# Optimization experiments

Hardware: AMD Instinct MI355X
Metric: run time of the kernel (lower is better)

## Reference

```python
import jax, jax.numpy as jnp
import numpy as np

DIM = 1024
NHEADS = 16
DIM_HEAD = 64
HIDDEN = NHEADS * DIM_HEAD  # 1024


def _xavier(key, fan_in, fan_out):
    limit = np.sqrt(6.0 / (fan_in + fan_out))
    return jax.random.uniform(key, (fan_in, fan_out), jnp.float32, -limit, limit)


def setup_inputs() -> dict:
    key = jax.random.key(0)
    kq, k1, k2, k3 = jax.random.split(key, 4)
    q = jax.random.normal(kq, (2, 2048, DIM), jnp.float32)
    Wq = _xavier(k1, DIM, HIDDEN)
    bq = jnp.zeros((HIDDEN,), jnp.float32)
    Wkv = _xavier(k2, DIM, 2 * HIDDEN)
    bkv = jnp.zeros((2 * HIDDEN,), jnp.float32)
    Wo = _xavier(k3, HIDDEN, DIM)
    bo = jnp.zeros((DIM,), jnp.float32)
    return {"q": q, "Wq": Wq, "bq": bq, "Wkv": Wkv, "bkv": bkv, "Wo": Wo, "bo": bo}


def reference(q, Wq, bq, Wkv, bkv, Wo, bo):
    scale = DIM_HEAD ** (-0.5)
    query = q @ Wq + bq                      # [b, s, hidden]
    kv = q @ Wkv + bkv                       # self-attention: kv from q
    key_, value = jnp.split(kv, 2, axis=-1)  # [b, s, hidden] each
    b, s, _ = query.shape
    query = query.reshape(b, s, NHEADS, DIM_HEAD)
    key_ = key_.reshape(b, s, NHEADS, DIM_HEAD)
    value = value.reshape(b, s, NHEADS, DIM_HEAD)
    scores = jnp.einsum('bqhd,bkhd->bhqk', query, key_) * scale
    attn = jax.nn.softmax(scores, axis=-1)
    out = jnp.einsum('bhqk,bkhd->bqhd', attn, value)
    out = out.reshape(b, s, HIDDEN)
    return out @ Wo + bo
```

## Files before the change

### kernel.cpp

```cpp
#include <hip/hip_runtime.h>

#define DIM 1024
#define NHEADS 16
#define DH 64
#define BATCH 2
#define SEQ 2048

typedef float f32x4 __attribute__((ext_vector_type(4)));
typedef short s16x8 __attribute__((ext_vector_type(8)));
typedef short s16x4 __attribute__((ext_vector_type(4)));

__device__ __forceinline__ short f2bf(float f) {
    union { float f; unsigned u; } v; v.f = f;
    unsigned r = v.u + 0x7fffu + ((v.u >> 16) & 1u);
    return (short)(r >> 16);
}

#if defined(__has_builtin)
#if __has_builtin(__builtin_amdgcn_cvt_pk_bf16_f32)
#define HAVE_PK_BF16 1
#endif
#endif
__device__ __forceinline__ unsigned f2bf_pk(float a, float b) {
#ifdef HAVE_PK_BF16
    typedef __bf16 bf16x2_t __attribute__((ext_vector_type(2)));
    bf16x2_t r = __builtin_amdgcn_cvt_pk_bf16_f32(a, b);
    return __builtin_bit_cast(unsigned, r);
#else
    return ((unsigned)(unsigned short)f2bf(b) << 16) | (unsigned short)f2bf(a);
#endif
}
__device__ __forceinline__ s16x4 pk4(float a, float b, float c, float d) {
    union { unsigned u[2]; s16x4 v; } x;
    x.u[0] = f2bf_pk(a, b); x.u[1] = f2bf_pk(c, d);
    return x.v;
}

#if defined(__has_builtin)
#if __has_builtin(__builtin_amdgcn_exp2f)
#define EXP2(x) __builtin_amdgcn_exp2f(x)
#endif
#endif
#ifndef EXP2
#define EXP2(x) exp2f(x)
#endif

__device__ __forceinline__ void gld16(const void* g, void* l) {
    __builtin_amdgcn_global_load_lds(
        (const __attribute__((address_space(1))) void*)g,
        (__attribute__((address_space(3))) void*)l, 16, 0, 0);
}

__global__ __launch_bounds__(256) void convert_bf16_kernel(
    const float* __restrict__ X, short* __restrict__ Y)
{
    const int i = (blockIdx.x * 256 + threadIdx.x) * 8;
    float4 a = *(const float4*)(X + i);
    float4 b = *(const float4*)(X + i + 4);
    union { unsigned u[4]; s16x8 v; } o;
    o.u[0] = f2bf_pk(a.x, a.y); o.u[1] = f2bf_pk(a.z, a.w);
    o.u[2] = f2bf_pk(b.x, b.y); o.u[3] = f2bf_pk(b.z, b.w);
    *(s16x8*)(Y + i) = o.v;
}

__global__ __launch_bounds__(256) void transpose_w_kernel(
    const float* __restrict__ Wq, const float* __restrict__ Wkv,
    const float* __restrict__ Wo, short* __restrict__ WT)
{
    const int t  = threadIdx.x;
    const int ng = blockIdx.x * 64 + (t & 63);
    const int k0 = (blockIdx.y * 4 + (t >> 6)) * 8;
    const float* W; int n, N;
    if (ng < 1024)      { W = Wq;  n = ng;        N = 1024; }
    else if (ng < 3072) { W = Wkv; n = ng - 1024; N = 2048; }
    else                { W = Wo;  n = ng - 3072; N = 1024; }
    float v[8];
#pragma unroll
    for (int j = 0; j < 8; ++j) v[j] = W[(size_t)(k0 + j) * N + n];
    union { unsigned u[4]; s16x8 s; } o;
    o.u[0] = f2bf_pk(v[0], v[1]); o.u[1] = f2bf_pk(v[2], v[3]);
    o.u[2] = f2bf_pk(v[4], v[5]); o.u[3] = f2bf_pk(v[6], v[7]);
    *(s16x8*)&WT[(size_t)ng * 1024 + k0] = o.s;
}

__global__ __launch_bounds__(256) void transpose_v_kernel(
    const short* __restrict__ QKV, short* __restrict__ VtG)
{
    const int t = threadIdx.x;
    const int tok0 = blockIdx.x * 64;
    const int h = blockIdx.y, b = blockIdx.z;
    __shared__ short L[64 * 72];
    const short* src = QKV + (size_t)(b * SEQ + tok0) * 3072 + 2048 + h * 64;
#pragma unroll
    for (int p = 0; p < 2; ++p) {
        int r = p * 32 + (t >> 3);
        *(s16x8*)&L[r * 72 + (t & 7) * 8] = *(const s16x8*)(src + (size_t)r * 3072 + (t & 7) * 8);
    }
    __syncthreads();
    short* dst = VtG + (size_t)(b * NHEADS + h) * 64 * SEQ + tok0;
#pragma unroll
    for (int p = 0; p < 2; ++p) {
        int u = p * 256 + t;
        int dv = u >> 3, c = (u & 7) * 8;
        s16x8 o;
#pragma unroll
        for (int j = 0; j < 8; ++j) o[j] = L[(c + j) * 72 + dv];
        *(s16x8*)(dst + (size_t)dv * SEQ + c) = o;
    }
}

template<int TM, bool OUT_BF16>
__global__ __launch_bounds__(256) void gemm_mfma_kernel(
    const short* __restrict__ A, const short* __restrict__ Bt,
    const float* __restrict__ bias0, const float* __restrict__ bias1, int nsplit,
    float s0, float s1, void* __restrict__ C, int M, int N)
{
    const int K = 1024;
    constexpr int NI = (TM == 128) ? 4 : 2;
    __shared__ short As[TM * 32];
    __shared__ short Bs[128 * 32];

    const int t    = threadIdx.x;
    const int wave = t >> 6;
    const int lane = t & 63;
    const int col  = lane & 15;
    const int quad = lane >> 4;
    const int m0 = blockIdx.y * TM;
    const int n0 = blockIdx.x * 128;
    const int wroff = (TM == 128) ? (wave >> 1) * 64 : 0;
    const int wcoff = (TM == 128) ? (wave & 1) * 64 : wave * 32;

    f32x4 acc[4][NI];
#pragma unroll
    for (int mi = 0; mi < 4; ++mi)
#pragma unroll
        for (int ni = 0; ni < NI; ++ni) acc[mi][ni] = (f32x4){0.f, 0.f, 0.f, 0.f};

    constexpr int RPW = TM / 4;
    const int ldrowA = wave * RPW + (lane >> 2);
    const int ldrowB = wave * 32  + (lane >> 2);
    const int ldcol  = (lane & 3) * 8;
    const short* Ag = A  + (size_t)(m0 + ldrowA) * K + ldcol;
    const short* Bg = Bt + (size_t)(n0 + ldrowB) * K + ldcol;
    short* AsW = &As[wave * RPW * 32];
    short* BsW = &Bs[wave * 1024];

    for (int k0 = 0; k0 < K; k0 += 32) {
        __syncthreads();
        gld16(Ag + k0, AsW);
        if (TM == 128) gld16(Ag + 16 * K + k0, AsW + 512);
        gld16(Bg + k0,          BsW);
        gld16(Bg + 16 * K + k0, BsW + 512);
        __syncthreads();

        s16x8 aA[4], bB[NI];
#pragma unroll
        for (int mi = 0; mi < 4; ++mi)
            aA[mi] = *(const s16x8*)&As[(wroff + 16 * mi + col) * 32 + quad * 8];
#pragma unroll
        for (int ni = 0; ni < NI; ++ni)
            bB[ni] = *(const s16x8*)&Bs[(wcoff + 16 * ni + col) * 32 + quad * 8];
#pragma unroll
        for (int mi = 0; mi < 4; ++mi)
#pragma unroll
            for (int ni = 0; ni < NI; ++ni)
                acc[mi][ni] = __builtin_amdgcn_mfma_f32_16x16x32_bf16(aA[mi], bB[ni], acc[mi][ni], 0, 0, 0);
    }

    float bias_v[NI], scale_v[NI];
#pragma unroll
    for (int ni = 0; ni < NI; ++ni) {
        int nb = n0 + wcoff + 16 * ni + col;
        bias_v[ni]  = (nb < nsplit) ? bias0[nb] : bias1[nb - nsplit];
        scale_v[ni] = (nb < nsplit) ? s0 : s1;
    }

#pragma unroll
    for (int mi = 0; mi < 4; ++mi)
#pragma unroll
        for (int ni = 0; ni < NI; ++ni)
#pragma unroll
            for (int r = 0; r < 4; ++r) {
                const int gm = m0 + wroff + 16 * mi + quad * 4 + r;
                const int gn = n0 + wcoff + 16 * ni + col;
                float v = (acc[mi][ni][r] + bias_v[ni]) * scale_v[ni];
                if (OUT_BF16) ((short*)C)[(size_t)gm * N + gn] = f2bf(v);
                else          ((float*)C)[(size_t)gm * N + gn] = v;
            }
}

__global__ __launch_bounds__(512, 4) void attn_v7_kernel(
    const short* __restrict__ QKV,
    const short* __restrict__ VtG,
    short* __restrict__ O)
{
    const int qt = blockIdx.x;
    const int h  = blockIdx.y;
    const int b  = blockIdx.z;
    const int t  = threadIdx.x;
    const int wave = t >> 6;
    const int lane = t & 63;
    const int col  = lane & 15;
    const int quad = lane >> 4;
    const int wq = wave & 3;
    const int kh = wave >> 2;

    __shared__ __align__(16) short L[28672];
    short* KsB = L;
    short* VtB = L + 2 * 64 * 72;
    short* PsW = L + 4 * 64 * 72 + wave * (32 * 40);

    const short* Qg = QKV + (size_t)(b * SEQ + qt * 128) * 3072 + h * DH;
    const short* Kg = QKV + (size_t)(b * SEQ) * 3072 + 1024 + h * DH;
    const short* VtRow = VtG + (size_t)(b * NHEADS + h) * 64 * SEQ;

    s16x8 aQ[2][2];
#pragma unroll
    for (int tq = 0; tq < 2; ++tq)
#pragma unroll
        for (int kq = 0; kq < 2; ++kq)
            aQ[tq][kq] = *(const s16x8*)(Qg + (size_t)(wq * 32 + 16 * tq + col) * 3072 + kq * 32 + quad * 8);

    f32x4 oa[4][2];
    float lsum[2] = {0.f, 0.f};
#pragma unroll
    for (int td = 0; td < 4; ++td)
#pragma unroll
        for (int tq = 0; tq < 2; ++tq) oa[td][tq] = (f32x4){0.f, 0.f, 0.f, 0.f};

    const int srow = t >> 3;
    const int sc8  = (t & 7) * 8;
    const short* KgS  = Kg + (size_t)srow * 3072 + sc8;
    const short* VtgS = VtRow + (size_t)srow * SEQ + sc8;
    s16x8 kx = *(const s16x8*)KgS;
    s16x8 vx = *(const s16x8*)VtgS;

    for (int kt = 0; kt < SEQ / 64; ++kt) {
        const int cur = kt & 1;
        *(s16x8*)&KsB[cur * 4608 + srow * 72 + sc8] = kx;
        *(s16x8*)&VtB[cur * 4608 + srow * 72 + sc8] = vx;
        {
            int nt = (kt + 1 < SEQ / 64) ? kt + 1 : kt;
            kx = *(const s16x8*)(KgS + (size_t)nt * 64 * 3072);
            vx = *(const s16x8*)(VtgS + (size_t)nt * 64);
        }
        __syncthreads();

        s16x8 aK[2][2];
#pragma unroll
        for (int tk = 0; tk < 2; ++tk)
#pragma unroll
            for (int kq = 0; kq < 2; ++kq)
                aK[tk][kq] = *(const s16x8*)&KsB[cur * 4608 + (kh * 32 + 16 * tk + col) * 72 + kq * 32 + quad * 8];
        f32x4 st[2][2];
        __builtin_amdgcn_s_setprio(1);
#pragma unroll
        for (int tk = 0; tk < 2; ++tk)
#pragma unroll
            for (int tq = 0; tq < 2; ++tq) {
                f32x4 a = (f32x4){0.f, 0.f, 0.f, 0.f};
                a = __builtin_amdgcn_mfma_f32_16x16x32_bf16(aK[tk][0], aQ[tq][0], a, 0, 0, 0);
                a = __builtin_amdgcn_mfma_f32_16x16x32_bf16(aK[tk][1], aQ[tq][1], a, 0, 0, 0);
                st[tk][tq] = a;
            }
        __builtin_amdgcn_s_setprio(0);

#pragma unroll
        for (int tk = 0; tk < 2; ++tk)
#pragma unroll
            for (int tq = 0; tq < 2; ++tq) {
                float p0 = EXP2(st[tk][tq][0]);
                float p1 = EXP2(st[tk][tq][1]);
                float p2 = EXP2(st[tk][tq][2]);
                float p3 = EXP2(st[tk][tq][3]);
                lsum[tq] += (p0 + p1) + (p2 + p3);
                *(s16x4*)&PsW[(16 * tq + col) * 40 + 16 * tk + quad * 4] = pk4(p0, p1, p2, p3);
            }
        asm volatile("s_waitcnt lgkmcnt(0)" ::: "memory");

        s16x8 bP[2];
#pragma unroll
        for (int tq = 0; tq < 2; ++tq)
            bP[tq] = *(const s16x8*)&PsW[(16 * tq + col) * 40 + quad * 8];
        __builtin_amdgcn_s_setprio(1);
#pragma unroll
        for (int td = 0; td < 4; ++td) {
            const int dv = 16 * td + col;
            s16x8 aV = *(const s16x8*)&VtB[cur * 4608 + dv * 72 + kh * 32 + quad * 8];
#pragma unroll
            for (int tq = 0; tq < 2; ++tq)
                oa[td][tq] = __builtin_amdgcn_mfma_f32_16x16x32_bf16(aV, bP[tq], oa[td][tq], 0, 0, 0);
        }
        __builtin_amdgcn_s_setprio(0);
    }

#pragma unroll
    for (int tq = 0; tq < 2; ++tq) {
        lsum[tq] += __shfl_xor(lsum[tq], 16);
        lsum[tq] += __shfl_xor(lsum[tq], 32);
    }

    __syncthreads();
    float* red  = (float*)L;
    float* redl = red + 4 * 64 * 36;
    if (wave >= 4) {
        const int slot = wave & 3;
#pragma unroll
        for (int td = 0; td < 4; ++td)
#pragma unroll
            for (int tq = 0; tq < 2; ++tq)
#pragma unroll
                for (int r = 0; r < 4; ++r)
                    red[slot * 2304 + (16 * td + quad * 4 + r) * 36 + 16 * tq + col] = oa[td][tq][r];
        if (quad == 0)
#pragma unroll
            for (int tq = 0; tq < 2; ++tq)
                redl[slot * 32 + 16 * tq + col] = lsum[tq];
    }
    __syncthreads();

    if (wave < 4) {
        const int slot = wq;
#pragma unroll
        for (int td = 0; td < 4; ++td)
#pragma unroll
            for (int tq = 0; tq < 2; ++tq)
#pragma unroll
                for (int r = 0; r < 4; ++r)
                    oa[td][tq][r] += red[slot * 2304 + (16 * td + quad * 4 + r) * 36 + 16 * tq + col];
        float inv[2];
#pragma unroll
        for (int tq = 0; tq < 2; ++tq) {
            lsum[tq] += redl[slot * 32 + 16 * tq + col];
            inv[tq] = 1.f / lsum[tq];
        }
        short* Og = O + (size_t)(b * SEQ + qt * 128 + wq * 32) * DIM + h * DH;
#pragma unroll
        for (int td = 0; td < 4; ++td)
#pragma unroll
            for (int tq = 0; tq < 2; ++tq)
                *(s16x4*)(Og + (size_t)(16 * tq + col) * DIM + 16 * td + quad * 4) =
                    pk4(oa[td][tq][0] * inv[tq], oa[td][tq][1] * inv[tq],
                        oa[td][tq][2] * inv[tq], oa[td][tq][3] * inv[tq]);
    }
}

extern "C" void kernel_launch(void* const* d_in, const int* in_sizes, int n_in,
                              void* d_out, int out_size, void* d_ws, size_t ws_size,
                              hipStream_t stream)
{
    const float* q   = (const float*)d_in[0];
    const float* Wq  = (const float*)d_in[1];
    const float* bq  = (const float*)d_in[2];
    const float* Wkv = (const float*)d_in[3];
    const float* bkv = (const float*)d_in[4];
    const float* Wo  = (const float*)d_in[5];
    const float* bo  = (const float*)d_in[6];
    float* out = (float*)d_out;

    const int M = BATCH * SEQ;

    short* qb     = (short*)d_ws;
    short* WT     = qb     + (size_t)M * DIM;
    short* QKVbuf = WT     + (size_t)4096 * DIM;
    short* AObuf  = QKVbuf + (size_t)M * 3 * DIM;
    short* VtG    = (short*)d_out;

    const float QSCALE = 0.18033688011112042f;

    convert_bf16_kernel<<<(M * DIM) / (256 * 8), 256, 0, stream>>>(q, qb);
    transpose_w_kernel<<<dim3(64, 32), 256, 0, stream>>>(Wq, Wkv, Wo, WT);

    gemm_mfma_kernel<128, true><<<dim3(3 * DIM / 128, M / 128), 256, 0, stream>>>(
        qb, WT, bq, bkv, DIM, QSCALE, 1.0f, QKVbuf, M, 3 * DIM);
    transpose_v_kernel<<<dim3(SEQ / 64, NHEADS, BATCH), 256, 0, stream>>>(QKVbuf, VtG);
    attn_v7_kernel<<<dim3(SEQ / 128, NHEADS, BATCH), 512, 0, stream>>>(QKVbuf, VtG, AObuf);
    gemm_mfma_kernel<64, false><<<dim3(DIM / 128, M / 64), 256, 0, stream>>>(
        AObuf, WT + (size_t)3072 * 1024, bo, bo, 1 << 30, 1.0f, 1.0f, out, M, DIM);
}
```

Baseline: 199.7 us.

## Fuse V transpose into QKV GEMM epilogue, merge prep kernels, remap attention blocks

Merges the input conversion and weight transpose into one prep kernel and removes the separate V-transpose kernel. The QKV GEMM epilogue now writes V columns straight into the transposed per-head layout with 4-element packed stores. The attention grid is remapped so each XCD handles a contiguous set of (batch, head) pairs, which is meant to improve L2 reuse of K/V. The goals are fewer launches, less global traffic, and better cache locality. The cost is strided transposed stores from the GEMM epilogue.

Result: slower. 203.8 us (+2.0%).

```diff
diff --git a/kernel.cpp b/kernel.cpp
--- a/kernel.cpp
+++ b/kernel.cpp
@@ -51,69 +51,44 @@
         (__attribute__((address_space(3))) void*)l, 16, 0, 0);
 }
 
-__global__ __launch_bounds__(256) void convert_bf16_kernel(
-    const float* __restrict__ X, short* __restrict__ Y)
-{
-    const int i = (blockIdx.x * 256 + threadIdx.x) * 8;
-    float4 a = *(const float4*)(X + i);
-    float4 b = *(const float4*)(X + i + 4);
-    union { unsigned u[4]; s16x8 v; } o;
-    o.u[0] = f2bf_pk(a.x, a.y); o.u[1] = f2bf_pk(a.z, a.w);
-    o.u[2] = f2bf_pk(b.x, b.y); o.u[3] = f2bf_pk(b.z, b.w);
-    *(s16x8*)(Y + i) = o.v;
-}
-
-__global__ __launch_bounds__(256) void transpose_w_kernel(
+__global__ __launch_bounds__(256) void prep_kernel(
+    const float* __restrict__ X, short* __restrict__ Y,
     const float* __restrict__ Wq, const float* __restrict__ Wkv,
     const float* __restrict__ Wo, short* __restrict__ WT)
 {
-    const int t  = threadIdx.x;
-    const int ng = blockIdx.x * 64 + (t & 63);
-    const int k0 = (blockIdx.y * 4 + (t >> 6)) * 8;
-    const float* W; int n, N;
-    if (ng < 1024)      { W = Wq;  n = ng;        N = 1024; }
-    else if (ng < 3072) { W = Wkv; n = ng - 1024; N = 2048; }
-    else                { W = Wo;  n = ng - 3072; N = 1024; }
-    float v[8];
-#pragma unroll
-    for (int j = 0; j < 8; ++j) v[j] = W[(size_t)(k0 + j) * N + n];
-    union { unsigned u[4]; s16x8 s; } o;
-    o.u[0] = f2bf_pk(v[0], v[1]); o.u[1] = f2bf_pk(v[2], v[3]);
-    o.u[2] = f2bf_pk(v[4], v[5]); o.u[3] = f2bf_pk(v[6], v[7]);
-    *(s16x8*)&WT[(size_t)ng * 1024 + k0] = o.s;
-}
-
-__global__ __launch_bounds__(256) void transpose_v_kernel(
-    const short* __restrict__ QKV, short* __restrict__ VtG)
-{
     const int t = threadIdx.x;
-    const int tok0 = blockIdx.x * 64;
-    const int h = blockIdx.y, b = blockIdx.z;
-    __shared__ short L[64 * 72];
-    const short* src = QKV + (size_t)(b * SEQ + tok0) * 3072 + 2048 + h * 64;
-#pragma unroll
-    for (int p = 0; p < 2; ++p) {
-        int r = p * 32 + (t >> 3);
-        *(s16x8*)&L[r * 72 + (t & 7) * 8] = *(const s16x8*)(src + (size_t)r * 3072 + (t & 7) * 8);
-    }
-    __syncthreads();
-    short* dst = VtG + (size_t)(b * NHEADS + h) * 64 * SEQ + tok0;
-#pragma unroll
-    for (int p = 0; p < 2; ++p) {
-        int u = p * 256 + t;
-        int dv = u >> 3, c = (u & 7) * 8;
-        s16x8 o;
-#pragma unroll
-        for (int j = 0; j < 8; ++j) o[j] = L[(c + j) * 72 + dv];
-        *(s16x8*)(dst + (size_t)dv * SEQ + c) = o;
-    }
-}
-
-template<int TM, bool OUT_BF16>
+    if (blockIdx.x < 2048) {
+        const int i = (blockIdx.x * 256 + t) * 8;
+        float4 a = *(const float4*)(X + i);
+        float4 b = *(const float4*)(X + i + 4);
+        union { unsigned u[4]; s16x8 v; } o;
+        o.u[0] = f2bf_pk(a.x, a.y); o.u[1] = f2bf_pk(a.z, a.w);
+        o.u[2] = f2bf_pk(b.x, b.y); o.u[3] = f2bf_pk(b.z, b.w);
+        *(s16x8*)(Y + i) = o.v;
+    } else {
+        const int i2 = blockIdx.x - 2048;
+        const int bx = i2 & 63, by = i2 >> 6;
+        const int ng = bx * 64 + (t & 63);
+        const int k0 = (by * 4 + (t >> 6)) * 8;
+        const float* W; int n, N;
+        if (ng < 1024)      { W = Wq;  n = ng;        N = 1024; }
+        else if (ng < 3072) { W = Wkv; n = ng - 1024; N = 2048; }
+        else                { W = Wo;  n = ng - 3072; N = 1024; }
+        float v[8];
+#pragma unroll
+        for (int j = 0; j < 8; ++j) v[j] = W[(size_t)(k0 + j) * N + n];
+        union { unsigned u[4]; s16x8 s; } o;
+        o.u[0] = f2bf_pk(v[0], v[1]); o.u[1] = f2bf_pk(v[2], v[3]);
+        o.u[2] = f2bf_pk(v[4], v[5]); o.u[3] = f2bf_pk(v[6], v[7]);
+        *(s16x8*)&WT[(size_t)ng * 1024 + k0] = o.s;
+    }
+}
+
+template<int TM, bool OUT_BF16, bool FUSE_V>
 __global__ __launch_bounds__(256) void gemm_mfma_kernel(
     const short* __restrict__ A, const short* __restrict__ Bt,
     const float* __restrict__ bias0, const float* __restrict__ bias1, int nsplit,
-    float s0, float s1, void* __restrict__ C, int M, int N)
+    float s0, float s1, void* __restrict__ C, short* __restrict__ VtGp, int M, int N)
 {
     const int K = 1024;
     constexpr int NI = (TM == 128) ? 4 : 2;
@@ -176,27 +151,44 @@
     }
 
 #pragma unroll
-    for (int mi = 0; mi < 4; ++mi)
-#pragma unroll
-        for (int ni = 0; ni < NI; ++ni)
-#pragma unroll
-            for (int r = 0; r < 4; ++r) {
-                const int gm = m0 + wroff + 16 * mi + quad * 4 + r;
-                const int gn = n0 + wcoff + 16 * ni + col;
-                float v = (acc[mi][ni][r] + bias_v[ni]) * scale_v[ni];
-                if (OUT_BF16) ((short*)C)[(size_t)gm * N + gn] = f2bf(v);
-                else          ((float*)C)[(size_t)gm * N + gn] = v;
+    for (int mi = 0; mi < 4; ++mi) {
+        const int gm0 = m0 + wroff + 16 * mi + quad * 4;
+#pragma unroll
+        for (int ni = 0; ni < NI; ++ni) {
+            const int nb_lo = n0 + wcoff + 16 * ni;
+            if (FUSE_V && nb_lo >= 2048) {
+                const int dv = nb_lo - 2048 + col;
+                float v0 = (acc[mi][ni][0] + bias_v[ni]) * scale_v[ni];
+                float v1 = (acc[mi][ni][1] + bias_v[ni]) * scale_v[ni];
+                float v2 = (acc[mi][ni][2] + bias_v[ni]) * scale_v[ni];
+                float v3 = (acc[mi][ni][3] + bias_v[ni]) * scale_v[ni];
+                const int row = ((gm0 >> 11) * NHEADS + (dv >> 6)) * 64 + (dv & 63);
+                *(s16x4*)&VtGp[(size_t)row * SEQ + (gm0 & 2047)] = pk4(v0, v1, v2, v3);
+            } else {
+#pragma unroll
+                for (int r = 0; r < 4; ++r) {
+                    const int gm = gm0 + r;
+                    const int gn = nb_lo + col;
+                    float v = (acc[mi][ni][r] + bias_v[ni]) * scale_v[ni];
+                    if (OUT_BF16) ((short*)C)[(size_t)gm * N + gn] = f2bf(v);
+                    else          ((float*)C)[(size_t)gm * N + gn] = v;
+                }
             }
-}
-
-__global__ __launch_bounds__(512, 4) void attn_v7_kernel(
+        }
+    }
+}
+
+__global__ __launch_bounds__(512, 4) void attn_v9_kernel(
     const short* __restrict__ QKV,
     const short* __restrict__ VtG,
     short* __restrict__ O)
 {
-    const int qt = blockIdx.x;
-    const int h  = blockIdx.y;
-    const int b  = blockIdx.z;
+    const int L = blockIdx.x + 16 * blockIdx.y + 256 * blockIdx.z;
+    const int xcd = L & 7, idx = L >> 3;
+    const int pair = xcd * 4 + (idx >> 4);
+    const int qt = idx & 15;
+    const int h  = pair & 15;
+    const int b  = pair >> 4;
     const int t  = threadIdx.x;
     const int wave = t >> 6;
     const int lane = t & 63;
@@ -205,10 +197,10 @@
     const int wq = wave & 3;
     const int kh = wave >> 2;
 
-    __shared__ __align__(16) short L[28672];
-    short* KsB = L;
-    short* VtB = L + 2 * 64 * 72;
-    short* PsW = L + 4 * 64 * 72 + wave * (32 * 40);
+    __shared__ __align__(16) short Lds[28672];
+    short* KsB = Lds;
+    short* VtB = Lds + 2 * 64 * 72;
+    short* PsW = Lds + 4 * 64 * 72 + wave * (32 * 40);
 
     const short* Qg = QKV + (size_t)(b * SEQ + qt * 128) * 3072 + h * DH;
     const short* Kg = QKV + (size_t)(b * SEQ) * 3072 + 1024 + h * DH;
@@ -301,7 +293,7 @@
     }
 
     __syncthreads();
-    float* red  = (float*)L;
+    float* red  = (float*)Lds;
     float* redl = red + 4 * 64 * 36;
     if (wave >= 4) {
         const int slot = wave & 3;
@@ -368,13 +360,11 @@
 
     const float QSCALE = 0.18033688011112042f;
 
-    convert_bf16_kernel<<<(M * DIM) / (256 * 8), 256, 0, stream>>>(q, qb);
-    transpose_w_kernel<<<dim3(64, 32), 256, 0, stream>>>(Wq, Wkv, Wo, WT);
-
-    gemm_mfma_kernel<128, true><<<dim3(3 * DIM / 128, M / 128), 256, 0, stream>>>(
-        qb, WT, bq, bkv, DIM, QSCALE, 1.0f, QKVbuf, M, 3 * DIM);
-    transpose_v_kernel<<<dim3(SEQ / 64, NHEADS, BATCH), 256, 0, stream>>>(QKVbuf, VtG);
-    attn_v7_kernel<<<dim3(SEQ / 128, NHEADS, BATCH), 512, 0, stream>>>(QKVbuf, VtG, AObuf);
-    gemm_mfma_kernel<64, false><<<dim3(DIM / 128, M / 64), 256, 0, stream>>>(
-        AObuf, WT + (size_t)3072 * 1024, bo, bo, 1 << 30, 1.0f, 1.0f, out, M, DIM);
-}
+    prep_kernel<<<4096, 256, 0, stream>>>(q, qb, Wq, Wkv, Wo, WT);
+
+    gemm_mfma_kernel<128, true, true><<<dim3(3 * DIM / 128, M / 128), 256, 0, stream>>>(
+        qb, WT, bq, bkv, DIM, QSCALE, 1.0f, QKVbuf, VtG, M, 3 * DIM);
+    attn_v9_kernel<<<dim3(SEQ / 128, NHEADS, BATCH), 512, 0, stream>>>(QKVbuf, VtG, AObuf);
+    gemm_mfma_kernel<64, false, false><<<dim3(DIM / 128, M / 64), 256, 0, stream>>>(
+        AObuf, WT + (size_t)3072 * 1024, bo, bo, 1 << 30, 1.0f, 1.0f, out, nullptr, M, DIM);
+}
```

## Fuse prep kernels, single-buffer attention LDS, raise occupancy, remap blocks per XCD

Applied to the files above, without the earlier changes.

The input conversion and weight transpose kernels are merged into one launch to save a kernel launch. The attention kernel drops double-buffered K/V LDS tiles and uses a single buffer guarded by two barriers per tile. This cuts LDS per block so launch bounds can ask for 8 waves per SIMD instead of 4. Block indices are remapped so that each XCD handles a contiguous set of (batch, head) pairs, which should improve L2 reuse of K/V, at the cost of the extra barrier per iteration and tighter register limits.

Result: slower. 434.3 us (+117.4%).

```diff
diff --git a/kernel.cpp b/kernel.cpp
--- a/kernel.cpp
+++ b/kernel.cpp
@@ -51,36 +51,37 @@
         (__attribute__((address_space(3))) void*)l, 16, 0, 0);
 }
 
-__global__ __launch_bounds__(256) void convert_bf16_kernel(
-    const float* __restrict__ X, short* __restrict__ Y)
-{
-    const int i = (blockIdx.x * 256 + threadIdx.x) * 8;
-    float4 a = *(const float4*)(X + i);
-    float4 b = *(const float4*)(X + i + 4);
-    union { unsigned u[4]; s16x8 v; } o;
-    o.u[0] = f2bf_pk(a.x, a.y); o.u[1] = f2bf_pk(a.z, a.w);
-    o.u[2] = f2bf_pk(b.x, b.y); o.u[3] = f2bf_pk(b.z, b.w);
-    *(s16x8*)(Y + i) = o.v;
-}
-
-__global__ __launch_bounds__(256) void transpose_w_kernel(
+__global__ __launch_bounds__(256) void prep_kernel(
+    const float* __restrict__ X, short* __restrict__ Y,
     const float* __restrict__ Wq, const float* __restrict__ Wkv,
     const float* __restrict__ Wo, short* __restrict__ WT)
 {
-    const int t  = threadIdx.x;
-    const int ng = blockIdx.x * 64 + (t & 63);
-    const int k0 = (blockIdx.y * 4 + (t >> 6)) * 8;
-    const float* W; int n, N;
-    if (ng < 1024)      { W = Wq;  n = ng;        N = 1024; }
-    else if (ng < 3072) { W = Wkv; n = ng - 1024; N = 2048; }
-    else                { W = Wo;  n = ng - 3072; N = 1024; }
-    float v[8];
-#pragma unroll
-    for (int j = 0; j < 8; ++j) v[j] = W[(size_t)(k0 + j) * N + n];
-    union { unsigned u[4]; s16x8 s; } o;
-    o.u[0] = f2bf_pk(v[0], v[1]); o.u[1] = f2bf_pk(v[2], v[3]);
-    o.u[2] = f2bf_pk(v[4], v[5]); o.u[3] = f2bf_pk(v[6], v[7]);
-    *(s16x8*)&WT[(size_t)ng * 1024 + k0] = o.s;
+    const int t = threadIdx.x;
+    if (blockIdx.x < 2048) {
+        const int i = (blockIdx.x * 256 + t) * 8;
+        float4 a = *(const float4*)(X + i);
+        float4 b = *(const float4*)(X + i + 4);
+        union { unsigned u[4]; s16x8 v; } o;
+        o.u[0] = f2bf_pk(a.x, a.y); o.u[1] = f2bf_pk(a.z, a.w);
+        o.u[2] = f2bf_pk(b.x, b.y); o.u[3] = f2bf_pk(b.z, b.w);
+        *(s16x8*)(Y + i) = o.v;
+    } else {
+        const int i2 = blockIdx.x - 2048;
+        const int bx = i2 & 63, by = i2 >> 6;
+        const int ng = bx * 64 + (t & 63);
+        const int k0 = (by * 4 + (t >> 6)) * 8;
+        const float* W; int n, N;
+        if (ng < 1024)      { W = Wq;  n = ng;        N = 1024; }
+        else if (ng < 3072) { W = Wkv; n = ng - 1024; N = 2048; }
+        else                { W = Wo;  n = ng - 3072; N = 1024; }
+        float v[8];
+#pragma unroll
+        for (int j = 0; j < 8; ++j) v[j] = W[(size_t)(k0 + j) * N + n];
+        union { unsigned u[4]; s16x8 s; } o;
+        o.u[0] = f2bf_pk(v[0], v[1]); o.u[1] = f2bf_pk(v[2], v[3]);
+        o.u[2] = f2bf_pk(v[4], v[5]); o.u[3] = f2bf_pk(v[6], v[7]);
+        *(s16x8*)&WT[(size_t)ng * 1024 + k0] = o.s;
+    }
 }
 
 __global__ __launch_bounds__(256) void transpose_v_kernel(
@@ -189,14 +190,17 @@
             }
 }
 
-__global__ __launch_bounds__(512, 4) void attn_v7_kernel(
+__global__ __launch_bounds__(512, 8) void attn_v10_kernel(
     const short* __restrict__ QKV,
     const short* __restrict__ VtG,
     short* __restrict__ O)
 {
-    const int qt = blockIdx.x;
-    const int h  = blockIdx.y;
-    const int b  = blockIdx.z;
+    const int L = blockIdx.x + 16 * blockIdx.y + 256 * blockIdx.z;
+    const int xcd = L & 7, idx = L >> 3;
+    const int pair = xcd * 4 + (idx >> 4);
+    const int qt = idx & 15;
+    const int h  = pair & 15;
+    const int b  = pair >> 4;
     const int t  = threadIdx.x;
     const int wave = t >> 6;
     const int lane = t & 63;
@@ -205,10 +209,10 @@
     const int wq = wave & 3;
     const int kh = wave >> 2;
 
-    __shared__ __align__(16) short L[28672];
-    short* KsB = L;
-    short* VtB = L + 2 * 64 * 72;
-    short* PsW = L + 4 * 64 * 72 + wave * (32 * 40);
+    __shared__ __align__(16) short Lds[19456];
+    short* Ks  = Lds;
+    short* Vt  = Lds + 4608;
+    short* PsW = Lds + 9216 + wave * (32 * 40);
 
     const short* Qg = QKV + (size_t)(b * SEQ + qt * 128) * 3072 + h * DH;
     const short* Kg = QKV + (size_t)(b * SEQ) * 3072 + 1024 + h * DH;
@@ -236,22 +240,22 @@
     s16x8 vx = *(const s16x8*)VtgS;
 
     for (int kt = 0; kt < SEQ / 64; ++kt) {
-        const int cur = kt & 1;
-        *(s16x8*)&KsB[cur * 4608 + srow * 72 + sc8] = kx;
-        *(s16x8*)&VtB[cur * 4608 + srow * 72 + sc8] = vx;
+        __syncthreads();
+        *(s16x8*)&Ks[srow * 72 + sc8] = kx;
+        *(s16x8*)&Vt[srow * 72 + sc8] = vx;
+        __syncthreads();
         {
             int nt = (kt + 1 < SEQ / 64) ? kt + 1 : kt;
             kx = *(const s16x8*)(KgS + (size_t)nt * 64 * 3072);
             vx = *(const s16x8*)(VtgS + (size_t)nt * 64);
         }
-        __syncthreads();
 
         s16x8 aK[2][2];
 #pragma unroll
         for (int tk = 0; tk < 2; ++tk)
 #pragma unroll
             for (int kq = 0; kq < 2; ++kq)
-                aK[tk][kq] = *(const s16x8*)&KsB[cur * 4608 + (kh * 32 + 16 * tk + col) * 72 + kq * 32 + quad * 8];
+                aK[tk][kq] = *(const s16x8*)&Ks[(kh * 32 + 16 * tk + col) * 72 + kq * 32 + quad * 8];
         f32x4 st[2][2];
         __builtin_amdgcn_s_setprio(1);
 #pragma unroll
@@ -286,7 +290,7 @@
 #pragma unroll
         for (int td = 0; td < 4; ++td) {
             const int dv = 16 * td + col;
-            s16x8 aV = *(const s16x8*)&VtB[cur * 4608 + dv * 72 + kh * 32 + quad * 8];
+            s16x8 aV = *(const s16x8*)&Vt[dv * 72 + kh * 32 + quad * 8];
 #pragma unroll
             for (int tq = 0; tq < 2; ++tq)
                 oa[td][tq] = __builtin_amdgcn_mfma_f32_16x16x32_bf16(aV, bP[tq], oa[td][tq], 0, 0, 0);
@@ -301,7 +305,7 @@
     }
 
     __syncthreads();
-    float* red  = (float*)L;
+    float* red  = (float*)Lds;
     float* redl = red + 4 * 64 * 36;
     if (wave >= 4) {
         const int slot = wave & 3;
@@ -368,13 +372,12 @@
 
     const float QSCALE = 0.18033688011112042f;
 
-    convert_bf16_kernel<<<(M * DIM) / (256 * 8), 256, 0, stream>>>(q, qb);
-    transpose_w_kernel<<<dim3(64, 32), 256, 0, stream>>>(Wq, Wkv, Wo, WT);
+    prep_kernel<<<4096, 256, 0, stream>>>(q, qb, Wq, Wkv, Wo, WT);
 
     gemm_mfma_kernel<128, true><<<dim3(3 * DIM / 128, M / 128), 256, 0, stream>>>(
         qb, WT, bq, bkv, DIM, QSCALE, 1.0f, QKVbuf, M, 3 * DIM);
     transpose_v_kernel<<<dim3(SEQ / 64, NHEADS, BATCH), 256, 0, stream>>>(QKVbuf, VtG);
-    attn_v7_kernel<<<dim3(SEQ / 128, NHEADS, BATCH), 512, 0, stream>>>(QKVbuf, VtG, AObuf);
+    attn_v10_kernel<<<dim3(SEQ / 128, NHEADS, BATCH), 512, 0, stream>>>(QKVbuf, VtG, AObuf);
     gemm_mfma_kernel<64, false><<<dim3(DIM / 128, M / 64), 256, 0, stream>>>(
         AObuf, WT + (size_t)3072 * 1024, bo, bo, 1 << 30, 1.0f, 1.0f, out, M, DIM);
 }
```
